# Kernel tuning notes

Measured on AMD Instinct MI355X. Metric: run time of the kernel, lower is better.

Reference implementation:

```python
import jax, jax.numpy as jnp
import numpy as np
from jax import lax

B, L, V, E, H = 256, 512, 256, 256, 1024


def setup_inputs() -> dict:
    key = jax.random.key(0)
    k1, k2, k3, k4, k5 = jax.random.split(key, 5)
    x = jax.random.randint(k1, (B, L), 0, V, dtype=jnp.int64)
    hidden = jnp.zeros((B, H), dtype=jnp.float32)
    emb_table = jax.random.normal(k2, (V, E), dtype=jnp.float32)  # nn.Embedding default init ~N(0,1)
    W_e = 0.01 * jax.random.normal(k3, (E, H), dtype=jnp.float32)
    W_h = 0.01 * jax.random.normal(k4, (H, H), dtype=jnp.float32)
    W_o = 0.01 * jax.random.normal(k5, (H, V), dtype=jnp.float32)
    return {"x": x, "hidden": hidden, "emb_table": emb_table, "W_e": W_e, "W_h": W_h, "W_o": W_o}


def reference(x, hidden, emb_table, W_e, W_h, W_o):
    # Precompute input projection for all timesteps in one batched GEMM:
    # emb_table[x] : [B, L, E];  x_proj : [L, B, H] (time-major for scan)
    x_proj = jnp.einsum('ble,eh->lbh', emb_table[x], W_e)

    def step(h_prev, x_t):
        h_t = jnp.tanh(x_t + h_prev @ W_h)  # [B, H]
        return h_t, h_t

    final_hidden, outs = lax.scan(step, hidden, x_proj)  # outs: [L, B, H]
    # logits: [B, L, V]
    logits = jnp.einsum('lbh,hv->blv', outs, W_o)
    return logits, final_hidden
```

## Files before the change

kernel.cpp:

```cpp
#include <hip/hip_runtime.h>
#include <hip/hip_bf16.h>
#include <math.h>

#define B_ 256
#define L_ 512
#define V_ 256
#define E_ 256
#define H_ 1024
#define NSTEP_ 513

typedef float  f32x4  __attribute__((ext_vector_type(4)));
typedef short  bf16x8 __attribute__((ext_vector_type(8)));

static __device__ __forceinline__ ushort f2bf(float v) {
    __hip_bfloat16 b = __float2bfloat16(v);
    return *reinterpret_cast<ushort*>(&b);
}

__global__ void k_transpose_bf16(const float* __restrict__ in, ushort* __restrict__ out,
                                 int R, int C) {
    __shared__ float tile[64][65];
    int bx = blockIdx.x;
    int by = blockIdx.y;
    int tid = threadIdx.x;
    int g = tid >> 6, l = tid & 63;
    for (int i = 0; i < 16; ++i) {
        int r = g * 16 + i;
        tile[r][l] = in[(size_t)(by * 64 + r) * C + bx * 64 + l];
    }
    __syncthreads();
    for (int i = 0; i < 16; ++i) {
        int c = g * 16 + i;
        out[(size_t)(bx * 64 + c) * R + by * 64 + l] = f2bf(tile[l][c]);
    }
}

__global__ void k_f32_to_bf16(const float* __restrict__ in, ushort* __restrict__ out, int n) {
    int i = blockIdx.x * blockDim.x + threadIdx.x;
    if (i < n) out[i] = f2bf(in[i]);
}

__global__ void k_zero(unsigned* __restrict__ p, int n) {
    int i = blockIdx.x * blockDim.x + threadIdx.x;
    if (i < n) p[i] = 0u;
}

__global__ void k_proj(const float* __restrict__ emb, const float* __restrict__ We,
                       float* __restrict__ proj) {
    __shared__ float er[E_];
    int t = blockIdx.x;
    int h = blockIdx.y * 256 + threadIdx.x;
    er[threadIdx.x] = emb[t * E_ + threadIdx.x];
    __syncthreads();
    float acc = 0.f;
#pragma unroll 8
    for (int e = 0; e < E_; ++e) acc += er[e] * We[(size_t)e * H_ + h];
    proj[(size_t)t * H_ + h] = acc;
}

__global__ __launch_bounds__(256, 1) void k_scan(
    const int* __restrict__ x, const float* __restrict__ proj,
    const ushort* __restrict__ WhT, const ushort* __restrict__ WoT,
    ushort* __restrict__ ring, float* __restrict__ logits,
    float* __restrict__ final_h, unsigned* __restrict__ flags)
{
    __shared__ ushort lds_w[32 * 1024];
    __shared__ ushort lds_h[32 * 1024];
    __shared__ float  red[256 * 5];
    __shared__ ushort stile[32 * 32];

    int tid = threadIdx.x;
    int w = tid >> 6, lane = tid & 63;
    int l15 = lane & 15, l4 = lane >> 4;
    int bid = blockIdx.x;
    int rg = bid & 7;
    int cg = bid >> 3;
    int r0 = rg * 32, c0 = cg * 32;

    {
        const char* wsrc = (const char*)(WhT + (size_t)c0 * H_);
        char* wd = (char*)lds_w;
        for (int i = 0; i < 16; ++i) {
            int chunk = (w * 16 + i) * 1024;
            int o = chunk + lane * 16;
            int row = o >> 11, b = o & 2047;
            int so = row * 2048 + (b ^ ((row & 7) << 4));
            __builtin_amdgcn_global_load_lds(
                (const __attribute__((address_space(1))) void*)(wsrc + so),
                (__attribute__((address_space(3))) void*)(wd + chunk), 16, 0, 0);
        }
    }

    int a = w >> 1, bc = w & 1;
    int arow = a * 16 + l15;
    int brow = bc * 16 + l15;
    const char* ha = (const char*)lds_h + arow * 2048;
    const char* wa = (const char*)lds_w + brow * 2048;
    int as = (arow & 7) << 4, bs = (brow & 7) << 4;
    int gcol = c0 + bc * 16 + l15;

    int lrg = cg & 1, vcol0 = (cg >> 1) * 16;
    int srow = lrg * 16 + l15;
    const char* hbp = (const char*)lds_h + srow * 2048;
    int hs2 = (srow & 7) << 4;
    const ushort* wo = WoT + (size_t)(vcol0 + l15) * H_;
    int bbase = (w == 1) ? 0 : (w == 2) ? 11 : 22;
    int bcnt  = (w == 3) ? 10 : 11;

    for (int s = 0; s <= NSTEP_; ++s) {
        float pv[4];
        if (s < L_) {
#pragma unroll
            for (int j = 0; j < 4; ++j) {
                int grow = r0 + a * 16 + l4 * 4 + j;
                pv[j] = proj[(size_t)x[grow * L_ + s] * H_ + gcol];
            }
        }

        if (w == 0) {
            if (s >= 1 && s <= L_) {
                const unsigned* fp = flags + ((size_t)rg * NSTEP_ + s) * 32 + lane;
                unsigned v = 1u;
                while (true) {
                    if (lane < 32) {
                        asm volatile("global_load_dword %0, %1, off sc0 sc1\n\t"
                                     "s_waitcnt vmcnt(0)"
                                     : "=v"(v) : "v"(fp) : "memory");
                    }
                    if (__ballot(v != 0u) == ~0ull) break;
                }
            }
        } else if (s >= 2) {
            f32x4 lacc = {0.f, 0.f, 0.f, 0.f};
            for (int kk = 0; kk < bcnt; ++kk) {
                int k = (bbase + kk) * 32 + l4 * 8;
                bf16x8 af = *(const bf16x8*)(hbp + ((2 * k) ^ hs2));
                bf16x8 bf = *(const bf16x8*)(wo + k);
                lacc = __builtin_amdgcn_mfma_f32_16x16x32_bf16(af, bf, lacc, 0, 0, 0);
            }
#pragma unroll
            for (int j = 0; j < 4; ++j) red[tid * 5 + j] = lacc[j];
        }
        __syncthreads();

        f32x4 tv[16];
        if (s <= L_) {
            const char* hsrc = (const char*)(ring + (size_t)(s & 1) * B_ * H_
                                             + (size_t)r0 * H_) + tid * 16;
#pragma unroll
            for (int i = 0; i < 16; ++i) {
                asm volatile("global_load_dwordx4 %0, %1, off sc0 sc1"
                             : "=v"(tv[i]) : "v"(hsrc + i * 4096) : "memory");
            }
        }
        if (w == 0 && s >= 2) {
            int growb = r0 + lrg * 16 + l4 * 4;
#pragma unroll
            for (int j = 0; j < 4; ++j) {
                float ssum = red[(64 + lane) * 5 + j] + red[(128 + lane) * 5 + j]
                           + red[(192 + lane) * 5 + j];
                logits[((size_t)(growb + j) * L_ + (s - 2)) * V_ + vcol0 + l15] = ssum;
            }
        }
        if (s <= L_) {
            asm volatile("s_waitcnt vmcnt(0)" ::: "memory");
#pragma unroll
            for (int i = 0; i < 16; ++i) {
                int o = i * 4096 + tid * 16;
                int row = o >> 11, b = o & 2047;
                *(f32x4*)((char*)lds_h + row * 2048 + (b ^ ((row & 7) << 4))) = tv[i];
            }
        }
        __syncthreads();

        if (s < L_) {
            f32x4 acc0 = {0.f, 0.f, 0.f, 0.f};
            f32x4 acc1 = {0.f, 0.f, 0.f, 0.f};
#pragma unroll
            for (int kk = 0; kk < 32; kk += 2) {
                int kb0 = (kk * 32 + l4 * 8) * 2;
                int kb1 = ((kk + 1) * 32 + l4 * 8) * 2;
                bf16x8 af0 = *(const bf16x8*)(ha + (kb0 ^ as));
                bf16x8 bf0 = *(const bf16x8*)(wa + (kb0 ^ bs));
                bf16x8 af1 = *(const bf16x8*)(ha + (kb1 ^ as));
                bf16x8 bf1 = *(const bf16x8*)(wa + (kb1 ^ bs));
                acc0 = __builtin_amdgcn_mfma_f32_16x16x32_bf16(af0, bf0, acc0, 0, 0, 0);
                acc1 = __builtin_amdgcn_mfma_f32_16x16x32_bf16(af1, bf1, acc1, 0, 0, 0);
            }
#pragma unroll
            for (int j = 0; j < 4; ++j) {
                int lrow = a * 16 + l4 * 4 + j;
                float hv = tanhf((acc0[j] + acc1[j]) + pv[j]);
                stile[lrow * 32 + bc * 16 + l15] = f2bf(hv);
                if (s == L_ - 1) final_h[(size_t)(r0 + lrow) * H_ + gcol] = hv;
            }
            __syncthreads();
            if (tid < 128) {
                int row = tid >> 2, seg = tid & 3;
                f32x4 d = *(const f32x4*)&stile[row * 32 + seg * 8];
                char* dst = (char*)(ring + (size_t)((s + 1) & 1) * B_ * H_
                                    + (size_t)(r0 + row) * H_ + c0 + seg * 8);
                asm volatile("global_store_dwordx4 %0, %1, off sc0 sc1"
                             :: "v"(dst), "v"(d) : "memory");
            }
            asm volatile("s_waitcnt vmcnt(0)" ::: "memory");
            __syncthreads();
            if (tid == 0) {
                unsigned* fdst = flags + ((size_t)rg * NSTEP_ + (s + 1)) * 32 + cg;
                unsigned one = 1u;
                asm volatile("global_store_dword %0, %1, off sc0 sc1"
                             :: "v"(fdst), "v"(one) : "memory");
            }
        }
    }
}

extern "C" void kernel_launch(void* const* d_in, const int* in_sizes, int n_in,
                              void* d_out, int out_size, void* d_ws, size_t ws_size,
                              hipStream_t stream)
{
    const int*   x   = (const int*)d_in[0];
    const float* hid = (const float*)d_in[1];
    const float* emb = (const float*)d_in[2];
    const float* We  = (const float*)d_in[3];
    const float* Wh  = (const float*)d_in[4];
    const float* Wo  = (const float*)d_in[5];

    float* logits  = (float*)d_out;
    float* final_h = logits + (size_t)B_ * L_ * V_;

    char* ws = (char*)d_ws;
    float*    proj  = (float*)(ws);
    ushort*   WhT   = (ushort*)(ws + (1u << 20));
    ushort*   WoT   = (ushort*)(ws + 3u * (1u << 20));
    ushort*   ring  = (ushort*)(ws + 3u * (1u << 20) + (1u << 19));
    unsigned* flags = (unsigned*)(ws + 4u * (1u << 20) + (1u << 19));

    k_zero<<<dim3(NSTEP_), 256, 0, stream>>>(flags, 8 * NSTEP_ * 32);
    k_transpose_bf16<<<dim3(16, 16), 256, 0, stream>>>(Wh, WhT, H_, H_);
    k_transpose_bf16<<<dim3(4, 16),  256, 0, stream>>>(Wo, WoT, H_, V_);
    k_f32_to_bf16<<<dim3(1024), 256, 0, stream>>>(hid, ring, B_ * H_);
    k_proj<<<dim3(256, 4), 256, 0, stream>>>(emb, We, proj);

    k_scan<<<dim3(256), 256, 0, stream>>>(x, proj, WhT, WoT, ring,
                                          logits, final_h, flags);
}
```

Baseline: 2.433 ms.

## Keep W_h slice in registers, double-buffer hidden state, overlap output GEMM with load

Each wave now loads its 16-column slice of W_h into 32 bf16x8 registers once, instead of staging it in LDS and re-reading it every step. The hidden-state LDS buffer is double-buffered, so the output-projection MFMAs for step s-2 can run while the ring load for step s is in flight, and one barrier per step goes away. tanhf is replaced with an exp-based fast tanh, and the staging tile row stride is padded to 40 to reduce LDS bank conflicts. The cost is much higher register pressure (128 VGPRs just for weights) and slightly lower tanh accuracy.

```diff
diff --git a/kernel.cpp b/kernel.cpp
--- a/kernel.cpp
+++ b/kernel.cpp
@@ -15,6 +15,11 @@
 static __device__ __forceinline__ ushort f2bf(float v) {
     __hip_bfloat16 b = __float2bfloat16(v);
     return *reinterpret_cast<ushort*>(&b);
+}
+
+static __device__ __forceinline__ float ftanh(float z) {
+    float e = __expf(2.f * z);
+    return 1.f - 2.f / (e + 1.f);
 }
 
 __global__ void k_transpose_bf16(const float* __restrict__ in, ushort* __restrict__ out,
@@ -64,10 +69,9 @@
     ushort* __restrict__ ring, float* __restrict__ logits,
     float* __restrict__ final_h, unsigned* __restrict__ flags)
 {
-    __shared__ ushort lds_w[32 * 1024];
-    __shared__ ushort lds_h[32 * 1024];
+    __shared__ ushort lds_h[2][32 * 1024];
     __shared__ float  red[256 * 5];
-    __shared__ ushort stile[32 * 32];
+    __shared__ ushort stile[32 * 40];
 
     int tid = threadIdx.x;
     int w = tid >> 6, lane = tid & 63;
@@ -77,31 +81,22 @@
     int cg = bid >> 3;
     int r0 = rg * 32, c0 = cg * 32;
 
-    {
-        const char* wsrc = (const char*)(WhT + (size_t)c0 * H_);
-        char* wd = (char*)lds_w;
-        for (int i = 0; i < 16; ++i) {
-            int chunk = (w * 16 + i) * 1024;
-            int o = chunk + lane * 16;
-            int row = o >> 11, b = o & 2047;
-            int so = row * 2048 + (b ^ ((row & 7) << 4));
-            __builtin_amdgcn_global_load_lds(
-                (const __attribute__((address_space(1))) void*)(wsrc + so),
-                (__attribute__((address_space(3))) void*)(wd + chunk), 16, 0, 0);
-        }
-    }
-
     int a = w >> 1, bc = w & 1;
     int arow = a * 16 + l15;
-    int brow = bc * 16 + l15;
-    const char* ha = (const char*)lds_h + arow * 2048;
-    const char* wa = (const char*)lds_w + brow * 2048;
-    int as = (arow & 7) << 4, bs = (brow & 7) << 4;
+    int as = (arow & 7) << 4;
     int gcol = c0 + bc * 16 + l15;
+
+    bf16x8 wreg[32];
+    {
+        const ushort* wp = WhT + (size_t)(c0 + bc * 16 + l15) * H_ + l4 * 8;
+#pragma unroll
+        for (int kk = 0; kk < 32; ++kk)
+            wreg[kk] = *(const bf16x8*)(wp + kk * 32);
+    }
 
     int lrg = cg & 1, vcol0 = (cg >> 1) * 16;
     int srow = lrg * 16 + l15;
-    const char* hbp = (const char*)lds_h + srow * 2048;
+    int sroff = srow * 2048;
     int hs2 = (srow & 7) << 4;
     const ushort* wo = WoT + (size_t)(vcol0 + l15) * H_;
     int bbase = (w == 1) ? 0 : (w == 2) ? 11 : 22;
@@ -117,20 +112,33 @@
             }
         }
 
-        if (w == 0) {
-            if (s >= 1 && s <= L_) {
-                const unsigned* fp = flags + ((size_t)rg * NSTEP_ + s) * 32 + lane;
-                unsigned v = 1u;
-                while (true) {
-                    if (lane < 32) {
-                        asm volatile("global_load_dword %0, %1, off sc0 sc1\n\t"
-                                     "s_waitcnt vmcnt(0)"
-                                     : "=v"(v) : "v"(fp) : "memory");
-                    }
-                    if (__ballot(v != 0u) == ~0ull) break;
+        if (w == 0 && s >= 1 && s <= L_) {
+            const unsigned* fp = flags + ((size_t)rg * NSTEP_ + s) * 32 + lane;
+            unsigned v = 1u;
+            while (true) {
+                if (lane < 32) {
+                    asm volatile("global_load_dword %0, %1, off sc0 sc1\n\t"
+                                 "s_waitcnt vmcnt(0)"
+                                 : "=v"(v) : "v"(fp) : "memory");
                 }
-            }
-        } else if (s >= 2) {
+                if (__ballot(v != 0u) == ~0ull) break;
+            }
+        }
+        __syncthreads();
+
+        f32x4 tv[16];
+        if (s <= L_) {
+            const char* hsrc = (const char*)(ring + (size_t)(s & 1) * B_ * H_
+                                             + (size_t)r0 * H_) + tid * 16;
+#pragma unroll
+            for (int i = 0; i < 16; ++i) {
+                asm volatile("global_load_dwordx4 %0, %1, off sc0 sc1"
+                             : "=v"(tv[i]) : "v"(hsrc + i * 4096) : "memory");
+            }
+        }
+
+        if (w >= 1 && s >= 2) {
+            const char* hbp = (const char*)lds_h[(s & 1) ^ 1] + sroff;
             f32x4 lacc = {0.f, 0.f, 0.f, 0.f};
             for (int kk = 0; kk < bcnt; ++kk) {
                 int k = (bbase + kk) * 32 + l4 * 8;
@@ -141,18 +149,19 @@
 #pragma unroll
             for (int j = 0; j < 4; ++j) red[tid * 5 + j] = lacc[j];
         }
+
+        if (s <= L_) {
+            asm volatile("s_waitcnt vmcnt(0)" ::: "memory");
+            char* hd = (char*)lds_h[s & 1];
+#pragma unroll
+            for (int i = 0; i < 16; ++i) {
+                int o = i * 4096 + tid * 16;
+                int row = o >> 11, b = o & 2047;
+                *(f32x4*)(hd + row * 2048 + (b ^ ((row & 7) << 4))) = tv[i];
+            }
+        }
         __syncthreads();
 
-        f32x4 tv[16];
-        if (s <= L_) {
-            const char* hsrc = (const char*)(ring + (size_t)(s & 1) * B_ * H_
-                                             + (size_t)r0 * H_) + tid * 16;
-#pragma unroll
-            for (int i = 0; i < 16; ++i) {
-                asm volatile("global_load_dwordx4 %0, %1, off sc0 sc1"
-                             : "=v"(tv[i]) : "v"(hsrc + i * 4096) : "memory");
-            }
-        }
         if (w == 0 && s >= 2) {
             int growb = r0 + lrg * 16 + l4 * 4;
 #pragma unroll
@@ -162,18 +171,9 @@
                 logits[((size_t)(growb + j) * L_ + (s - 2)) * V_ + vcol0 + l15] = ssum;
             }
         }
-        if (s <= L_) {
-            asm volatile("s_waitcnt vmcnt(0)" ::: "memory");
-#pragma unroll
-            for (int i = 0; i < 16; ++i) {
-                int o = i * 4096 + tid * 16;
-                int row = o >> 11, b = o & 2047;
-                *(f32x4*)((char*)lds_h + row * 2048 + (b ^ ((row & 7) << 4))) = tv[i];
-            }
-        }
-        __syncthreads();
 
         if (s < L_) {
+            const char* ha = (const char*)lds_h[s & 1] + arow * 2048;
             f32x4 acc0 = {0.f, 0.f, 0.f, 0.f};
             f32x4 acc1 = {0.f, 0.f, 0.f, 0.f};
 #pragma unroll
@@ -181,23 +181,21 @@
                 int kb0 = (kk * 32 + l4 * 8) * 2;
                 int kb1 = ((kk + 1) * 32 + l4 * 8) * 2;
                 bf16x8 af0 = *(const bf16x8*)(ha + (kb0 ^ as));
-                bf16x8 bf0 = *(const bf16x8*)(wa + (kb0 ^ bs));
                 bf16x8 af1 = *(const bf16x8*)(ha + (kb1 ^ as));
-                bf16x8 bf1 = *(const bf16x8*)(wa + (kb1 ^ bs));
-                acc0 = __builtin_amdgcn_mfma_f32_16x16x32_bf16(af0, bf0, acc0, 0, 0, 0);
-                acc1 = __builtin_amdgcn_mfma_f32_16x16x32_bf16(af1, bf1, acc1, 0, 0, 0);
+                acc0 = __builtin_amdgcn_mfma_f32_16x16x32_bf16(af0, wreg[kk],     acc0, 0, 0, 0);
+                acc1 = __builtin_amdgcn_mfma_f32_16x16x32_bf16(af1, wreg[kk + 1], acc1, 0, 0, 0);
             }
 #pragma unroll
             for (int j = 0; j < 4; ++j) {
                 int lrow = a * 16 + l4 * 4 + j;
-                float hv = tanhf((acc0[j] + acc1[j]) + pv[j]);
-                stile[lrow * 32 + bc * 16 + l15] = f2bf(hv);
+                float hv = ftanh((acc0[j] + acc1[j]) + pv[j]);
+                stile[lrow * 40 + bc * 16 + l15] = f2bf(hv);
                 if (s == L_ - 1) final_h[(size_t)(r0 + lrow) * H_ + gcol] = hv;
             }
             __syncthreads();
             if (tid < 128) {
                 int row = tid >> 2, seg = tid & 3;
-                f32x4 d = *(const f32x4*)&stile[row * 32 + seg * 8];
+                f32x4 d = *(const f32x4*)&stile[row * 40 + seg * 8];
                 char* dst = (char*)(ring + (size_t)((s + 1) & 1) * B_ * H_
                                     + (size_t)(r0 + row) * H_ + c0 + seg * 8);
                 asm volatile("global_store_dwordx4 %0, %1, off sc0 sc1"
```

Measured after the change: 2.613 ms. 1.07x slower.

## Replace flag-based inter-block sync with step-tagged hidden-state words in ring

Applied to the files above, without the earlier changes.

Drops the separate flag array and its poll/store handshake. Each bf16 hidden value is now packed with a 16-bit step tag in a 32-bit word, and consumers spin-load the ring until every tag matches the current step. This removes the store-drain, barrier and flag-store round trip on every timestep, at the cost of doubling ring traffic. The output projection is moved after the recurrence and split evenly across all four waves, and tanhf is replaced by an exp-based fast tanh.

```diff
diff --git a/kernel.cpp b/kernel.cpp
--- a/kernel.cpp
+++ b/kernel.cpp
@@ -7,21 +7,27 @@
 #define V_ 256
 #define E_ 256
 #define H_ 1024
-#define NSTEP_ 513
 
 typedef float  f32x4  __attribute__((ext_vector_type(4)));
 typedef short  bf16x8 __attribute__((ext_vector_type(8)));
+typedef unsigned int u32;
+typedef unsigned int u32x2 __attribute__((ext_vector_type(2)));
+typedef unsigned int u32x4 __attribute__((ext_vector_type(4)));
 
 static __device__ __forceinline__ ushort f2bf(float v) {
     __hip_bfloat16 b = __float2bfloat16(v);
     return *reinterpret_cast<ushort*>(&b);
 }
 
+static __device__ __forceinline__ float ftanh(float z) {
+    float e = __expf(2.f * z);
+    return 1.f - 2.f / (e + 1.f);
+}
+
 __global__ void k_transpose_bf16(const float* __restrict__ in, ushort* __restrict__ out,
                                  int R, int C) {
     __shared__ float tile[64][65];
-    int bx = blockIdx.x;
-    int by = blockIdx.y;
+    int bx = blockIdx.x, by = blockIdx.y;
     int tid = threadIdx.x;
     int g = tid >> 6, l = tid & 63;
     for (int i = 0; i < 16; ++i) {
@@ -35,14 +41,14 @@
     }
 }
 
-__global__ void k_f32_to_bf16(const float* __restrict__ in, ushort* __restrict__ out, int n) {
-    int i = blockIdx.x * blockDim.x + threadIdx.x;
-    if (i < n) out[i] = f2bf(in[i]);
-}
-
-__global__ void k_zero(unsigned* __restrict__ p, int n) {
+__global__ void k_zero(u32* __restrict__ p, int n) {
     int i = blockIdx.x * blockDim.x + threadIdx.x;
     if (i < n) p[i] = 0u;
+}
+
+__global__ void k_pack0(const float* __restrict__ hid, u32* __restrict__ ring, int n) {
+    int i = blockIdx.x * blockDim.x + threadIdx.x;
+    if (i < n) ring[i] = ((u32)f2bf(hid[i]) << 16) | 0u;
 }
 
 __global__ void k_proj(const float* __restrict__ emb, const float* __restrict__ We,
@@ -61,13 +67,12 @@
 __global__ __launch_bounds__(256, 1) void k_scan(
     const int* __restrict__ x, const float* __restrict__ proj,
     const ushort* __restrict__ WhT, const ushort* __restrict__ WoT,
-    ushort* __restrict__ ring, float* __restrict__ logits,
-    float* __restrict__ final_h, unsigned* __restrict__ flags)
+    u32* __restrict__ ring, float* __restrict__ logits,
+    float* __restrict__ final_h)
 {
     __shared__ ushort lds_w[32 * 1024];
-    __shared__ ushort lds_h[32 * 1024];
+    __shared__ ushort panel[32 * 1024];
     __shared__ float  red[256 * 5];
-    __shared__ ushort stile[32 * 32];
 
     int tid = threadIdx.x;
     int w = tid >> 6, lane = tid & 63;
@@ -94,20 +99,18 @@
     int a = w >> 1, bc = w & 1;
     int arow = a * 16 + l15;
     int brow = bc * 16 + l15;
-    const char* ha = (const char*)lds_h + arow * 2048;
+    const char* ha = (const char*)panel + arow * 2048;
     const char* wa = (const char*)lds_w + brow * 2048;
     int as = (arow & 7) << 4, bs = (brow & 7) << 4;
     int gcol = c0 + bc * 16 + l15;
 
     int lrg = cg & 1, vcol0 = (cg >> 1) * 16;
     int srow = lrg * 16 + l15;
-    const char* hbp = (const char*)lds_h + srow * 2048;
+    const char* hbp = (const char*)panel + srow * 2048;
     int hs2 = (srow & 7) << 4;
     const ushort* wo = WoT + (size_t)(vcol0 + l15) * H_;
-    int bbase = (w == 1) ? 0 : (w == 2) ? 11 : 22;
-    int bcnt  = (w == 3) ? 10 : 11;
-
-    for (int s = 0; s <= NSTEP_; ++s) {
+
+    for (int s = 0; s <= L_; ++s) {
         float pv[4];
         if (s < L_) {
 #pragma unroll
@@ -117,58 +120,38 @@
             }
         }
 
-        if (w == 0) {
-            if (s >= 1 && s <= L_) {
-                const unsigned* fp = flags + ((size_t)rg * NSTEP_ + s) * 32 + lane;
-                unsigned v = 1u;
-                while (true) {
-                    if (lane < 32) {
-                        asm volatile("global_load_dword %0, %1, off sc0 sc1\n\t"
-                                     "s_waitcnt vmcnt(0)"
-                                     : "=v"(v) : "v"(fp) : "memory");
+        {
+            const u32 tag = (u32)s;
+            const char* base = (const char*)(ring + (size_t)(s & 1) * B_ * H_
+                                             + (size_t)r0 * H_);
+            for (int c = 0; c < 2; ++c) {
+                u32x4 tv[16];
+                bool ok;
+                do {
+#pragma unroll
+                    for (int i = 0; i < 16; ++i) {
+                        const char* p = base + (size_t)(c * 16 + i) * 4096 + tid * 16;
+                        asm volatile("global_load_dwordx4 %0, %1, off sc0 sc1"
+                                     : "=v"(tv[i]) : "v"(p) : "memory");
                     }
-                    if (__ballot(v != 0u) == ~0ull) break;
+                    asm volatile("s_waitcnt vmcnt(0)" ::: "memory");
+                    __builtin_amdgcn_sched_barrier(0);
+                    ok = true;
+#pragma unroll
+                    for (int i = 0; i < 16; ++i)
+#pragma unroll
+                        for (int j = 0; j < 4; ++j)
+                            ok = ok & ((tv[i][j] & 0xFFFFu) == tag);
+                } while (!ok);
+#pragma unroll
+                for (int i = 0; i < 16; ++i) {
+                    u32 lo = (tv[i][1] & 0xFFFF0000u) | (tv[i][0] >> 16);
+                    u32 hi = (tv[i][3] & 0xFFFF0000u) | (tv[i][2] >> 16);
+                    int row = c * 16 + i;
+                    int b = tid * 8;
+                    int o = row * 2048 + (b ^ ((row & 7) << 4));
+                    *(u32x2*)((char*)panel + o) = (u32x2){lo, hi};
                 }
-            }
-        } else if (s >= 2) {
-            f32x4 lacc = {0.f, 0.f, 0.f, 0.f};
-            for (int kk = 0; kk < bcnt; ++kk) {
-                int k = (bbase + kk) * 32 + l4 * 8;
-                bf16x8 af = *(const bf16x8*)(hbp + ((2 * k) ^ hs2));
-                bf16x8 bf = *(const bf16x8*)(wo + k);
-                lacc = __builtin_amdgcn_mfma_f32_16x16x32_bf16(af, bf, lacc, 0, 0, 0);
-            }
-#pragma unroll
-            for (int j = 0; j < 4; ++j) red[tid * 5 + j] = lacc[j];
-        }
-        __syncthreads();
-
-        f32x4 tv[16];
-        if (s <= L_) {
-            const char* hsrc = (const char*)(ring + (size_t)(s & 1) * B_ * H_
-                                             + (size_t)r0 * H_) + tid * 16;
-#pragma unroll
-            for (int i = 0; i < 16; ++i) {
-                asm volatile("global_load_dwordx4 %0, %1, off sc0 sc1"
-                             : "=v"(tv[i]) : "v"(hsrc + i * 4096) : "memory");
-            }
-        }
-        if (w == 0 && s >= 2) {
-            int growb = r0 + lrg * 16 + l4 * 4;
-#pragma unroll
-            for (int j = 0; j < 4; ++j) {
-                float ssum = red[(64 + lane) * 5 + j] + red[(128 + lane) * 5 + j]
-                           + red[(192 + lane) * 5 + j];
-                logits[((size_t)(growb + j) * L_ + (s - 2)) * V_ + vcol0 + l15] = ssum;
-            }
-        }
-        if (s <= L_) {
-            asm volatile("s_waitcnt vmcnt(0)" ::: "memory");
-#pragma unroll
-            for (int i = 0; i < 16; ++i) {
-                int o = i * 4096 + tid * 16;
-                int row = o >> 11, b = o & 2047;
-                *(f32x4*)((char*)lds_h + row * 2048 + (b ^ ((row & 7) << 4))) = tv[i];
             }
         }
         __syncthreads();
@@ -187,31 +170,42 @@
                 acc0 = __builtin_amdgcn_mfma_f32_16x16x32_bf16(af0, bf0, acc0, 0, 0, 0);
                 acc1 = __builtin_amdgcn_mfma_f32_16x16x32_bf16(af1, bf1, acc1, 0, 0, 0);
             }
+            u32* rdst = ring + (size_t)((s + 1) & 1) * B_ * H_;
 #pragma unroll
             for (int j = 0; j < 4; ++j) {
-                int lrow = a * 16 + l4 * 4 + j;
-                float hv = tanhf((acc0[j] + acc1[j]) + pv[j]);
-                stile[lrow * 32 + bc * 16 + l15] = f2bf(hv);
-                if (s == L_ - 1) final_h[(size_t)(r0 + lrow) * H_ + gcol] = hv;
-            }
+                int grow = r0 + a * 16 + l4 * 4 + j;
+                float hv = ftanh((acc0[j] + acc1[j]) + pv[j]);
+                u32 word = ((u32)f2bf(hv) << 16) | (u32)(s + 1);
+                u32* dst = rdst + (size_t)grow * H_ + gcol;
+                asm volatile("global_store_dword %0, %1, off sc0 sc1"
+                             :: "v"(dst), "v"(word) : "memory");
+                if (s == L_ - 1) final_h[(size_t)grow * H_ + gcol] = hv;
+            }
+        }
+
+        if (s >= 1) {
+            f32x4 lacc = {0.f, 0.f, 0.f, 0.f};
+#pragma unroll
+            for (int kk = 0; kk < 8; ++kk) {
+                int k = w * 256 + kk * 32 + l4 * 8;
+                bf16x8 af = *(const bf16x8*)(hbp + ((2 * k) ^ hs2));
+                bf16x8 bf = *(const bf16x8*)(wo + k);
+                lacc = __builtin_amdgcn_mfma_f32_16x16x32_bf16(af, bf, lacc, 0, 0, 0);
+            }
+#pragma unroll
+            for (int j = 0; j < 4; ++j) red[tid * 5 + j] = lacc[j];
             __syncthreads();
-            if (tid < 128) {
-                int row = tid >> 2, seg = tid & 3;
-                f32x4 d = *(const f32x4*)&stile[row * 32 + seg * 8];
-                char* dst = (char*)(ring + (size_t)((s + 1) & 1) * B_ * H_
-                                    + (size_t)(r0 + row) * H_ + c0 + seg * 8);
-                asm volatile("global_store_dwordx4 %0, %1, off sc0 sc1"
-                             :: "v"(dst), "v"(d) : "memory");
-            }
-            asm volatile("s_waitcnt vmcnt(0)" ::: "memory");
-            __syncthreads();
-            if (tid == 0) {
-                unsigned* fdst = flags + ((size_t)rg * NSTEP_ + (s + 1)) * 32 + cg;
-                unsigned one = 1u;
-                asm volatile("global_store_dword %0, %1, off sc0 sc1"
-                             :: "v"(fdst), "v"(one) : "memory");
-            }
-        }
+            if (w == 0) {
+                int growb = r0 + lrg * 16 + l4 * 4;
+#pragma unroll
+                for (int j = 0; j < 4; ++j) {
+                    float ssum = red[(0 * 64 + lane) * 5 + j] + red[(64 + lane) * 5 + j]
+                               + red[(128 + lane) * 5 + j] + red[(192 + lane) * 5 + j];
+                    logits[((size_t)(growb + j) * L_ + (s - 1)) * V_ + vcol0 + l15] = ssum;
+                }
+            }
+        }
+        __syncthreads();
     }
 }
 
@@ -230,18 +224,18 @@
     float* final_h = logits + (size_t)B_ * L_ * V_;
 
     char* ws = (char*)d_ws;
-    float*    proj  = (float*)(ws);
-    ushort*   WhT   = (ushort*)(ws + (1u << 20));
-    ushort*   WoT   = (ushort*)(ws + 3u * (1u << 20));
-    ushort*   ring  = (ushort*)(ws + 3u * (1u << 20) + (1u << 19));
-    unsigned* flags = (unsigned*)(ws + 4u * (1u << 20) + (1u << 19));
-
-    k_zero<<<dim3(NSTEP_), 256, 0, stream>>>(flags, 8 * NSTEP_ * 32);
+    float*  proj = (float*)(ws);
+    ushort* WhT  = (ushort*)(ws + (1u << 20));
+    ushort* WoT  = (ushort*)(ws + 3u * (1u << 20));
+    u32*    ring = (u32*)(ws + 3u * (1u << 20) + (1u << 19));
+
+    const int RN = 2 * B_ * H_;
+    k_zero<<<dim3(RN / 256), 256, 0, stream>>>(ring, RN);
     k_transpose_bf16<<<dim3(16, 16), 256, 0, stream>>>(Wh, WhT, H_, H_);
     k_transpose_bf16<<<dim3(4, 16),  256, 0, stream>>>(Wo, WoT, H_, V_);
-    k_f32_to_bf16<<<dim3(1024), 256, 0, stream>>>(hid, ring, B_ * H_);
+    k_pack0<<<dim3(B_ * H_ / 256), 256, 0, stream>>>(hid, ring, B_ * H_);
     k_proj<<<dim3(256, 4), 256, 0, stream>>>(emb, We, proj);
 
     k_scan<<<dim3(256), 256, 0, stream>>>(x, proj, WhT, WoT, ring,
-                                          logits, final_h, flags);
-}
+                                          logits, final_h);
+}
```

New measurement: 3.009 ms. +23.7%, slower.

## Split batch into two interleaved halves to overlap recurrence latency across phases

Applied to the files above, without the earlier changes.

The batch is split into two independent halves, each with its own hidden-state ring and flag set. The scan loop alternates phases between them, so one half's store, flag signalling and output projection overlap with the other half's load and recurrent matmul. Work is also reassigned: two waves compute the recurrence for 16 rows while two waves compute the logits. Flags become bytes, tanh is replaced by an exp-based form, and the per-step number of barriers is reduced. The trade-offs are twice as many grid-wide flag handshakes per timestep and a tanh that is slightly less accurate.

```diff
diff --git a/kernel.cpp b/kernel.cpp
--- a/kernel.cpp
+++ b/kernel.cpp
@@ -7,21 +7,26 @@
 #define V_ 256
 #define E_ 256
 #define H_ 1024
-#define NSTEP_ 513
 
 typedef float  f32x4  __attribute__((ext_vector_type(4)));
 typedef short  bf16x8 __attribute__((ext_vector_type(8)));
+typedef unsigned int u32;
+typedef unsigned char u8;
 
 static __device__ __forceinline__ ushort f2bf(float v) {
     __hip_bfloat16 b = __float2bfloat16(v);
     return *reinterpret_cast<ushort*>(&b);
 }
 
+static __device__ __forceinline__ float ftanh(float z) {
+    float e = __expf(2.f * z);
+    return 1.f - 2.f / (e + 1.f);
+}
+
 __global__ void k_transpose_bf16(const float* __restrict__ in, ushort* __restrict__ out,
                                  int R, int C) {
     __shared__ float tile[64][65];
-    int bx = blockIdx.x;
-    int by = blockIdx.y;
+    int bx = blockIdx.x, by = blockIdx.y;
     int tid = threadIdx.x;
     int g = tid >> 6, l = tid & 63;
     for (int i = 0; i < 16; ++i) {
@@ -35,14 +40,18 @@
     }
 }
 
-__global__ void k_f32_to_bf16(const float* __restrict__ in, ushort* __restrict__ out, int n) {
-    int i = blockIdx.x * blockDim.x + threadIdx.x;
-    if (i < n) out[i] = f2bf(in[i]);
-}
-
-__global__ void k_zero(unsigned* __restrict__ p, int n) {
+__global__ void k_zero(u32* __restrict__ p, int n) {
     int i = blockIdx.x * blockDim.x + threadIdx.x;
     if (i < n) p[i] = 0u;
+}
+
+__global__ void k_pack_h0(const float* __restrict__ hid, ushort* __restrict__ ringA,
+                          ushort* __restrict__ ringB) {
+    int i = blockIdx.x * blockDim.x + threadIdx.x;
+    ushort v = f2bf(hid[i]);
+    int half = i >> 17;
+    int off = i & 131071;
+    if (half == 0) ringA[off] = v; else ringB[off] = v;
 }
 
 __global__ void k_proj(const float* __restrict__ emb, const float* __restrict__ We,
@@ -59,23 +68,23 @@
 }
 
 __global__ __launch_bounds__(256, 1) void k_scan(
-    const int* __restrict__ x, const float* __restrict__ proj,
+    const int* __restrict__ xs, const float* __restrict__ proj,
     const ushort* __restrict__ WhT, const ushort* __restrict__ WoT,
-    ushort* __restrict__ ring, float* __restrict__ logits,
-    float* __restrict__ final_h, unsigned* __restrict__ flags)
+    ushort* __restrict__ ringA, ushort* __restrict__ ringB,
+    float* __restrict__ logits, float* __restrict__ final_h,
+    u8* __restrict__ flags)
 {
     __shared__ ushort lds_w[32 * 1024];
-    __shared__ ushort lds_h[32 * 1024];
-    __shared__ float  red[256 * 5];
-    __shared__ ushort stile[32 * 32];
+    __shared__ ushort panel[16 * 1024];
+    __shared__ float  red[2][16][17];
+    __shared__ ushort stile[16 * 32];
 
     int tid = threadIdx.x;
     int w = tid >> 6, lane = tid & 63;
     int l15 = lane & 15, l4 = lane >> 4;
     int bid = blockIdx.x;
-    int rg = bid & 7;
-    int cg = bid >> 3;
-    int r0 = rg * 32, c0 = cg * 32;
+    int rg = bid & 7, cg = bid >> 3;
+    int c0 = cg * 32;
 
     {
         const char* wsrc = (const char*)(WhT + (size_t)c0 * H_);
@@ -91,127 +100,133 @@
         }
     }
 
-    int a = w >> 1, bc = w & 1;
-    int arow = a * 16 + l15;
-    int brow = bc * 16 + l15;
-    const char* ha = (const char*)lds_h + arow * 2048;
-    const char* wa = (const char*)lds_w + brow * 2048;
-    int as = (arow & 7) << 4, bs = (brow & 7) << 4;
-    int gcol = c0 + bc * 16 + l15;
-
-    int lrg = cg & 1, vcol0 = (cg >> 1) * 16;
-    int srow = lrg * 16 + l15;
-    const char* hbp = (const char*)lds_h + srow * 2048;
-    int hs2 = (srow & 7) << 4;
+    int as = (l15 & 7) << 4;
+    const char* wa = (const char*)lds_w + (size_t)((w & 1) * 16 + l15) * 2048;
+    int vcol0 = (cg & 15) * 16;
     const ushort* wo = WoT + (size_t)(vcol0 + l15) * H_;
-    int bbase = (w == 1) ? 0 : (w == 2) ? 11 : 22;
-    int bcnt  = (w == 3) ? 10 : 11;
-
-    for (int s = 0; s <= NSTEP_; ++s) {
-        float pv[4];
-        if (s < L_) {
-#pragma unroll
-            for (int j = 0; j < 4; ++j) {
-                int grow = r0 + a * 16 + l4 * 4 + j;
-                pv[j] = proj[(size_t)x[grow * L_ + s] * H_ + gcol];
-            }
-        }
-
-        if (w == 0) {
-            if (s >= 1 && s <= L_) {
-                const unsigned* fp = flags + ((size_t)rg * NSTEP_ + s) * 32 + lane;
-                unsigned v = 1u;
-                while (true) {
-                    if (lane < 32) {
-                        asm volatile("global_load_dword %0, %1, off sc0 sc1\n\t"
-                                     "s_waitcnt vmcnt(0)"
-                                     : "=v"(v) : "v"(fp) : "memory");
-                    }
-                    if (__ballot(v != 0u) == ~0ull) break;
-                }
-            }
-        } else if (s >= 2) {
-            f32x4 lacc = {0.f, 0.f, 0.f, 0.f};
-            for (int kk = 0; kk < bcnt; ++kk) {
-                int k = (bbase + kk) * 32 + l4 * 8;
-                bf16x8 af = *(const bf16x8*)(hbp + ((2 * k) ^ hs2));
-                bf16x8 bf = *(const bf16x8*)(wo + k);
-                lacc = __builtin_amdgcn_mfma_f32_16x16x32_bf16(af, bf, lacc, 0, 0, 0);
-            }
-#pragma unroll
-            for (int j = 0; j < 4; ++j) red[tid * 5 + j] = lacc[j];
+
+    for (int p = 0; p <= 2 * L_ + 2; ++p) {
+        int hx = p & 1, s = p >> 1;
+        int px = (p - 1) & 1, ps = (p - 1) >> 1;
+        bool doStage = (p <= 2 * L_ + 1);
+        bool doPoll = doStage && (s >= 1);
+
+        ushort* ringR = hx ? ringB : ringA;
+
+        if (w == 0 && doPoll) {
+            const u8* fp = flags + ((size_t)(hx * 8 + rg) * 513 + s) * 32 + lane;
+            u32 v = 1u;
+            while (true) {
+                if (lane < 32)
+                    asm volatile("global_load_ubyte %0, %1, off sc0 sc1\n\t"
+                                 "s_waitcnt vmcnt(0)" : "=v"(v) : "v"(fp) : "memory");
+                if (__ballot(v != 0u) == ~0ull) break;
+            }
         }
         __syncthreads();
 
-        f32x4 tv[16];
-        if (s <= L_) {
-            const char* hsrc = (const char*)(ring + (size_t)(s & 1) * B_ * H_
-                                             + (size_t)r0 * H_) + tid * 16;
-#pragma unroll
-            for (int i = 0; i < 16; ++i) {
+        f32x4 tv[8];
+        if (doStage) {
+            const char* hsrc = (const char*)(ringR + (size_t)(s & 1) * 128 * H_
+                                             + (size_t)(rg * 16) * H_) + tid * 16;
+#pragma unroll
+            for (int i = 0; i < 8; ++i)
                 asm volatile("global_load_dwordx4 %0, %1, off sc0 sc1"
                              : "=v"(tv[i]) : "v"(hsrc + i * 4096) : "memory");
-            }
-        }
-        if (w == 0 && s >= 2) {
-            int growb = r0 + lrg * 16 + l4 * 4;
+        }
+
+        if (p >= 1) {
+            if (w == 0 && ps < L_) {
+                ushort* ringW = px ? ringB : ringA;
+                int r = lane >> 2, seg = lane & 3;
+                f32x4 d = *(const f32x4*)&stile[r * 32 + seg * 8];
+                char* dst = (char*)(ringW + (size_t)((ps + 1) & 1) * 128 * H_
+                                    + (size_t)(rg * 16 + r) * H_ + c0 + seg * 8);
+                asm volatile("global_store_dwordx4 %0, %1, off sc0 sc1"
+                             :: "v"(dst), "v"(d) : "memory");
+                asm volatile("s_waitcnt vmcnt(0)" ::: "memory");
+                if (lane == 0) {
+                    u8* fdst = flags + ((size_t)(px * 8 + rg) * 513 + (ps + 1)) * 32 + cg;
+                    u32 one = 1u;
+                    asm volatile("global_store_byte %0, %1, off sc0 sc1"
+                                 :: "v"(fdst), "v"(one) : "memory");
+                }
+            }
+            if (w == 2 && ps >= 1 && cg < 16) {
+                int r = lane >> 2, c4 = (lane & 3) * 4;
+                f32x4 o;
+#pragma unroll
+                for (int j = 0; j < 4; ++j) o[j] = red[0][r][c4 + j] + red[1][r][c4 + j];
+                int grow = px * 128 + rg * 16 + r;
+                *(f32x4*)&logits[((size_t)grow * L_ + (ps - 1)) * V_ + vcol0 + c4] = o;
+            }
+        }
+
+        float pv[4];
+        if (w < 2 && doStage && s < L_) {
 #pragma unroll
             for (int j = 0; j < 4; ++j) {
-                float ssum = red[(64 + lane) * 5 + j] + red[(128 + lane) * 5 + j]
-                           + red[(192 + lane) * 5 + j];
-                logits[((size_t)(growb + j) * L_ + (s - 2)) * V_ + vcol0 + l15] = ssum;
-            }
-        }
-        if (s <= L_) {
+                int grow = hx * 128 + rg * 16 + l4 * 4 + j;
+                pv[j] = proj[(size_t)xs[grow * L_ + s] * H_ + c0 + w * 16 + l15];
+            }
+        }
+
+        if (doStage) {
             asm volatile("s_waitcnt vmcnt(0)" ::: "memory");
 #pragma unroll
-            for (int i = 0; i < 16; ++i) {
+            for (int i = 0; i < 8; ++i) {
                 int o = i * 4096 + tid * 16;
                 int row = o >> 11, b = o & 2047;
-                *(f32x4*)((char*)lds_h + row * 2048 + (b ^ ((row & 7) << 4))) = tv[i];
+                *(f32x4*)((char*)panel + row * 2048 + (b ^ ((row & 7) << 4))) = tv[i];
             }
         }
         __syncthreads();
 
-        if (s < L_) {
-            f32x4 acc0 = {0.f, 0.f, 0.f, 0.f};
-            f32x4 acc1 = {0.f, 0.f, 0.f, 0.f};
+        if (w < 2 && doStage && s < L_) {
+            const char* ha = (const char*)panel + l15 * 2048;
+            f32x4 acc0 = {0.f,0.f,0.f,0.f}, acc1 = {0.f,0.f,0.f,0.f};
 #pragma unroll
             for (int kk = 0; kk < 32; kk += 2) {
                 int kb0 = (kk * 32 + l4 * 8) * 2;
                 int kb1 = ((kk + 1) * 32 + l4 * 8) * 2;
                 bf16x8 af0 = *(const bf16x8*)(ha + (kb0 ^ as));
-                bf16x8 bf0 = *(const bf16x8*)(wa + (kb0 ^ bs));
+                bf16x8 bf0 = *(const bf16x8*)(wa + (kb0 ^ as));
                 bf16x8 af1 = *(const bf16x8*)(ha + (kb1 ^ as));
-                bf16x8 bf1 = *(const bf16x8*)(wa + (kb1 ^ bs));
+                bf16x8 bf1 = *(const bf16x8*)(wa + (kb1 ^ as));
                 acc0 = __builtin_amdgcn_mfma_f32_16x16x32_bf16(af0, bf0, acc0, 0, 0, 0);
                 acc1 = __builtin_amdgcn_mfma_f32_16x16x32_bf16(af1, bf1, acc1, 0, 0, 0);
             }
 #pragma unroll
             for (int j = 0; j < 4; ++j) {
-                int lrow = a * 16 + l4 * 4 + j;
-                float hv = tanhf((acc0[j] + acc1[j]) + pv[j]);
-                stile[lrow * 32 + bc * 16 + l15] = f2bf(hv);
-                if (s == L_ - 1) final_h[(size_t)(r0 + lrow) * H_ + gcol] = hv;
-            }
-            __syncthreads();
-            if (tid < 128) {
-                int row = tid >> 2, seg = tid & 3;
-                f32x4 d = *(const f32x4*)&stile[row * 32 + seg * 8];
-                char* dst = (char*)(ring + (size_t)((s + 1) & 1) * B_ * H_
-                                    + (size_t)(r0 + row) * H_ + c0 + seg * 8);
-                asm volatile("global_store_dwordx4 %0, %1, off sc0 sc1"
-                             :: "v"(dst), "v"(d) : "memory");
-            }
-            asm volatile("s_waitcnt vmcnt(0)" ::: "memory");
-            __syncthreads();
-            if (tid == 0) {
-                unsigned* fdst = flags + ((size_t)rg * NSTEP_ + (s + 1)) * 32 + cg;
-                unsigned one = 1u;
-                asm volatile("global_store_dword %0, %1, off sc0 sc1"
-                             :: "v"(fdst), "v"(one) : "memory");
-            }
-        }
+                int lrow = l4 * 4 + j;
+                float hv = ftanh((acc0[j] + acc1[j]) + pv[j]);
+                stile[lrow * 32 + w * 16 + l15] = f2bf(hv);
+                if (s == L_ - 1) {
+                    int grow = hx * 128 + rg * 16 + lrow;
+                    final_h[(size_t)grow * H_ + c0 + w * 16 + l15] = hv;
+                }
+            }
+        }
+
+        if (w >= 2 && doStage && s >= 1 && cg < 16) {
+            const char* ha = (const char*)panel + l15 * 2048;
+            int kh = w - 2;
+            f32x4 acc0 = {0.f,0.f,0.f,0.f}, acc1 = {0.f,0.f,0.f,0.f};
+#pragma unroll
+            for (int kk = 0; kk < 16; kk += 2) {
+                int k0 = kh * 512 + kk * 32 + l4 * 8;
+                int k1 = k0 + 32;
+                bf16x8 a0 = *(const bf16x8*)(ha + ((2 * k0) ^ as));
+                bf16x8 b0 = *(const bf16x8*)(wo + k0);
+                bf16x8 a1 = *(const bf16x8*)(ha + ((2 * k1) ^ as));
+                bf16x8 b1 = *(const bf16x8*)(wo + k1);
+                acc0 = __builtin_amdgcn_mfma_f32_16x16x32_bf16(a0, b0, acc0, 0, 0, 0);
+                acc1 = __builtin_amdgcn_mfma_f32_16x16x32_bf16(a1, b1, acc1, 0, 0, 0);
+            }
+#pragma unroll
+            for (int j = 0; j < 4; ++j) red[kh][l4 * 4 + j][l15] = acc0[j] + acc1[j];
+        }
+        __syncthreads();
     }
 }
 
@@ -230,18 +245,20 @@
     float* final_h = logits + (size_t)B_ * L_ * V_;
 
     char* ws = (char*)d_ws;
-    float*    proj  = (float*)(ws);
-    ushort*   WhT   = (ushort*)(ws + (1u << 20));
-    ushort*   WoT   = (ushort*)(ws + 3u * (1u << 20));
-    ushort*   ring  = (ushort*)(ws + 3u * (1u << 20) + (1u << 19));
-    unsigned* flags = (unsigned*)(ws + 4u * (1u << 20) + (1u << 19));
-
-    k_zero<<<dim3(NSTEP_), 256, 0, stream>>>(flags, 8 * NSTEP_ * 32);
+    float*  proj  = (float*)(ws);
+    ushort* WhT   = (ushort*)(ws + (1u << 20));
+    ushort* WoT   = (ushort*)(ws + 3u * (1u << 20));
+    ushort* ringA = (ushort*)(ws + 3u * (1u << 20) + (1u << 19));
+    ushort* ringB = (ushort*)(ws + 4u * (1u << 20));
+    u8*     flags = (u8*)(ws + 4u * (1u << 20) + (1u << 19));
+
+    const int FN = 2 * 8 * 513 * 32 / 4;
+    k_zero<<<dim3((FN + 255) / 256), 256, 0, stream>>>((u32*)flags, FN);
     k_transpose_bf16<<<dim3(16, 16), 256, 0, stream>>>(Wh, WhT, H_, H_);
     k_transpose_bf16<<<dim3(4, 16),  256, 0, stream>>>(Wo, WoT, H_, V_);
-    k_f32_to_bf16<<<dim3(1024), 256, 0, stream>>>(hid, ring, B_ * H_);
+    k_pack_h0<<<dim3(B_ * H_ / 256), 256, 0, stream>>>(hid, ringA, ringB);
     k_proj<<<dim3(256, 4), 256, 0, stream>>>(emb, We, proj);
 
-    k_scan<<<dim3(256), 256, 0, stream>>>(x, proj, WhT, WoT, ring,
+    k_scan<<<dim3(256), 256, 0, stream>>>(x, proj, WhT, WoT, ringA, ringB,
                                           logits, final_h, flags);
 }
```

Result: no change. 2.461 ms (+1.2%).
